# Optimization experiments

Hardware: AMD Instinct MI355X
Metric: run time of the kernel (lower is better)

The kernel has to match this reference:

```python
import jax, jax.numpy as jnp
import numpy as np

STEPS, K, NEW_PTS, GDIM, HDIM = 10, 64, 1152, 256, 128


def setup_inputs() -> dict:
    key = jax.random.key(0)
    ks = jax.random.split(key, 24)
    def w(k, shape):
        return jax.random.normal(k, shape, dtype=jnp.float32) * 0.02
    inp = {
        'points': jax.random.normal(ks[0], (4, 4096, 3), dtype=jnp.float32),
        'gt': jax.random.normal(ks[1], (4, 4096, 3), dtype=jnp.float32),
        # PointNet encoder: 3->64->128->256 (stored [in,out])
        'enc_w1': w(ks[2], (3, 64)),   'enc_b1': jnp.zeros((64,), jnp.float32),
        'enc_w2': w(ks[3], (64, 128)), 'enc_b2': jnp.zeros((128,), jnp.float32),
        'enc_w3': w(ks[4], (128, GDIM)), 'enc_b3': jnp.zeros((GDIM,), jnp.float32),
        # Attention MLP: (3+256+128)->128->1
        'att_w1': w(ks[5], (3 + GDIM + HDIM, 128)), 'att_b1': jnp.zeros((128,), jnp.float32),
        'att_w2': w(ks[6], (128, 1)), 'att_b2': jnp.zeros((1,), jnp.float32),
        # LSTMCell: input 256+3+3=262, hidden 128, gates i,f,g,o
        'lstm_wih': w(ks[7], (GDIM + 6, 4 * HDIM)), 'lstm_whh': w(ks[8], (HDIM, 4 * HDIM)),
        'lstm_bih': jnp.zeros((4 * HDIM,), jnp.float32), 'lstm_bhh': jnp.zeros((4 * HDIM,), jnp.float32),
        # Refiner: 128->128->new_points*3
        'ref_w1': w(ks[9], (HDIM, 128)), 'ref_b1': jnp.zeros((128,), jnp.float32),
        'ref_w2': w(ks[10], (128, NEW_PTS * 3)), 'ref_b2': jnp.zeros((NEW_PTS * 3,), jnp.float32),
    }
    return inp


def _chamfer_sq(x, y):
    # x: [B,N,3], y: [B,M,3]; squared-L2 chamfer, batch-mean (pytorch3d norm=2)
    d2 = (jnp.sum(x * x, -1)[:, :, None] + jnp.sum(y * y, -1)[:, None, :]
          - 2.0 * jnp.einsum('bnd,bmd->bnm', x, y))  # [B,N,M]
    cd = jnp.mean(jnp.min(d2, axis=2), axis=1) + jnp.mean(jnp.min(d2, axis=1), axis=1)
    return jnp.mean(cd)


def _forward(points, gt, enc_w1, enc_b1, enc_w2, enc_b2, enc_w3, enc_b3,
             att_w1, att_b1, att_w2, att_b2,
             lstm_wih, lstm_whh, lstm_bih, lstm_bhh,
             ref_w1, ref_b1, ref_w2, ref_b2):
    B, N0, _ = points.shape
    h = jnp.zeros((B, HDIM), points.dtype)
    c = jnp.zeros((B, HDIM), points.dtype)
    canvas = points
    for _ in range(STEPS):
        # PointNet encoder + max-pool -> global feature [B,GDIM]
        f = jax.nn.relu(canvas @ enc_w1 + enc_b1)
        f = jax.nn.relu(f @ enc_w2 + enc_b2)
        f = f @ enc_w3 + enc_b3
        gfeat = jnp.max(f, axis=1)
        # attention-weighted centroid
        N = canvas.shape[1]
        ctx = jnp.concatenate([
            canvas,
            jnp.broadcast_to(gfeat[:, None, :], (B, N, GDIM)),
            jnp.broadcast_to(h[:, None, :], (B, N, HDIM)),
        ], axis=-1)
        scores = (jax.nn.relu(ctx @ att_w1 + att_b1) @ att_w2 + att_b2)[..., 0]  # [B,N]
        alpha = jax.nn.softmax(scores, axis=1)
        center = jnp.einsum('bn,bnd->bd', alpha, canvas)
        # brute-force KNN around center + gather
        dist = jnp.linalg.norm(canvas - center[:, None, :], axis=-1)  # [B,N]
        _, idx = jax.lax.top_k(-dist, K)  # smallest K
        patch = jnp.take_along_axis(canvas, idx[:, :, None], axis=1)  # [B,K,3]
        patch_feat = jnp.mean(patch - center[:, None, :], axis=1)  # [B,3]
        # LSTM cell (gate order i,f,g,o)
        lstm_in = jnp.concatenate([gfeat, center, patch_feat], axis=1)
        gates = lstm_in @ lstm_wih + lstm_bih + h @ lstm_whh + lstm_bhh
        gi, gf, gg, go = jnp.split(gates, 4, axis=1)
        c = jax.nn.sigmoid(gf) * c + jax.nn.sigmoid(gi) * jnp.tanh(gg)
        h = jax.nn.sigmoid(go) * jnp.tanh(c)
        # refine: generate new patch points around center
        new_pts = (jax.nn.relu(h @ ref_w1 + ref_b1) @ ref_w2 + ref_b2)
        new_pts = new_pts.reshape(B, NEW_PTS, 3) * 0.02 + center[:, None, :]
        canvas = jnp.concatenate([canvas, new_pts], axis=1)
    p_input = canvas[:, :N0, :]
    p_new = canvas[:, N0:, :]
    total_loss = 0.1 * _chamfer_sq(p_input, gt) + 1.0 * _chamfer_sq(p_new, gt)
    return total_loss


def reference(points, gt, enc_w1, enc_b1, enc_w2, enc_b2, enc_w3, enc_b3,
              att_w1, att_b1, att_w2, att_b2,
              lstm_wih, lstm_whh, lstm_bih, lstm_bhh,
              ref_w1, ref_b1, ref_w2, ref_b2):
    return _forward(points, gt, enc_w1, enc_b1, enc_w2, enc_b2, enc_w3, enc_b3,
                    att_w1, att_b1, att_w2, att_b2,
                    lstm_wih, lstm_whh, lstm_bih, lstm_bhh,
                    ref_w1, ref_b1, ref_w2, ref_b2)
```

## Files before the change

### kernel.cpp

```cpp
#include <hip/hip_runtime.h>
#include <math.h>

#define BB 4
#define N0 4096
#define NEWP 1152
#define GD 256
#define HD 128
#define KSEL 64
#define NSTEPS 10
#define NMAX (N0 + NSTEPS*NEWP)
#define NNEW (NSTEPS*NEWP)
#define F2S (BB*N0)

#define OFF_CANVAS 0
#define OFF_MINAB  (OFF_CANVAS + BB*NMAX*3)
#define OFF_MINCD  (OFF_MINAB + 2*BB*N0)
#define OFF_GMAX   (OFF_MINCD + BB*NNEW + BB*N0)
#define OFF_H      (OFF_GMAX + BB*GD)
#define OFF_C      (OFF_H + 2*BB*HD)
#define OFF_ACC    (OFF_C + 2*BB*HD)
#define OFF_CENTER (OFF_ACC + 16)
#define OFF_PART   (OFF_CENTER + 32)
#define OFF_GPART  (OFF_PART + BB*32*8)
#define OFF_F2     (OFF_GPART + 32*BB*512)
#define WS_FLOATS  (OFF_F2 + 128*F2S)

__device__ __forceinline__ unsigned enc_f(float f){
  unsigned u = __float_as_uint(f);
  return (u & 0x80000000u) ? ~u : (u | 0x80000000u);
}
__device__ __forceinline__ float dec_f(unsigned e){
  unsigned u = (e & 0x80000000u) ? (e & 0x7fffffffu) : ~e;
  return __uint_as_float(u);
}
__device__ __forceinline__ float sigm(float x){ return 1.f/(1.f+expf(-x)); }

__device__ __forceinline__ float block_sum(float v, volatile float* red){
#pragma unroll
  for (int s=32;s>0;s>>=1) v += __shfl_down(v, s, 64);
  int lane = threadIdx.x & 63, w = threadIdx.x >> 6, nw = blockDim.x >> 6;
  __syncthreads();
  if (lane==0) red[w] = v;
  __syncthreads();
  if (w==0){
    float x = (lane < nw) ? red[lane] : 0.f;
#pragma unroll
    for (int s=8;s>0;s>>=1) x += __shfl_down(x, s, 64);
    if (lane==0) red[0] = x;
  }
  __syncthreads();
  float r = red[0];
  __syncthreads();
  return r;
}
__device__ __forceinline__ float block_max(float v, volatile float* red){
#pragma unroll
  for (int s=32;s>0;s>>=1) v = fmaxf(v, __shfl_down(v, s, 64));
  int lane = threadIdx.x & 63, w = threadIdx.x >> 6, nw = blockDim.x >> 6;
  __syncthreads();
  if (lane==0) red[w] = v;
  __syncthreads();
  if (w==0){
    float x = (lane < nw) ? red[lane] : -3.4e38f;
#pragma unroll
    for (int s=8;s>0;s>>=1) x = fmaxf(x, __shfl_down(x, s, 64));
    if (lane==0) red[0] = x;
  }
  __syncthreads();
  float r = red[0];
  __syncthreads();
  return r;
}

__global__ __launch_bounds__(512) void init_kernel(
    const float* __restrict__ points,
    float* __restrict__ canvas, unsigned* __restrict__ minAB,
    unsigned* __restrict__ minCD, unsigned* __restrict__ gmax,
    float* __restrict__ h, float* __restrict__ c)
{
  int gid = blockIdx.x*512 + threadIdx.x;
  if (gid < BB*N0*3){
    int b = gid/(N0*3), r = gid - b*(N0*3);
    canvas[(size_t)b*NMAX*3 + r] = points[gid];
  }
  if (gid < 2*BB*N0) minAB[gid] = 0xFFFFFFFFu;
  if (gid < BB*NNEW + BB*N0) minCD[gid] = 0xFFFFFFFFu;
  if (gid < BB*GD) gmax[gid] = 0u;
  if (gid < 2*BB*HD){ h[gid]=0.f; c[gid]=0.f; }
}

__global__ __launch_bounds__(256) void enc12_kernel(
    const float* __restrict__ canvas, const float* __restrict__ w1,
    const float* __restrict__ b1, const float* __restrict__ w2,
    const float* __restrict__ b2, float* __restrict__ f2buf,
    int off, int M)
{
  int b = blockIdx.y;
  int jc = blockIdx.z;
  int i = blockIdx.x*256 + threadIdx.x;
  int ii = (i < M) ? i : 0;
  const float* p = canvas + (size_t)(b*NMAX + off + ii)*3;
  float p0 = p[0], p1 = p[1], p2 = p[2];
  float f1[64];
#pragma unroll
  for (int j=0;j<64;j++)
    f1[j] = fmaxf(0.f, b1[j] + p0*w1[j] + p1*w1[64+j] + p2*w1[128+j]);
  float a[16];
  const float* b2p = b2 + jc*16;
#pragma unroll
  for (int j=0;j<16;j++) a[j] = b2p[j];
#pragma unroll
  for (int k=0;k<64;k++){
    const float* wr = w2 + k*128 + jc*16;
#pragma unroll
    for (int j=0;j<16;j++) a[j] = fmaf(f1[k], wr[j], a[j]);
  }
  if (i < M){
    int base = b*N0 + i;
#pragma unroll
    for (int j=0;j<16;j++)
      f2buf[(size_t)(jc*16 + j)*F2S + base] = fmaxf(a[j], 0.f);
  }
}

__global__ __launch_bounds__(256) void enc3_kernel(
    const float* __restrict__ f2buf, const float* __restrict__ w3,
    const float* __restrict__ b3, unsigned* __restrict__ gmax, int M)
{
  int b = blockIdx.y;
  int dc = blockIdx.z;
  int i = blockIdx.x*256 + threadIdx.x;
  bool act = i < M;
  int ii = act ? i : 0;
  const float* fp = f2buf + b*N0 + ii;
  float a[16];
  const float* b3p = b3 + dc*16;
#pragma unroll
  for (int d=0;d<16;d++) a[d] = b3p[d];
  for (int k=0;k<128;k++){
    float fk = fp[(size_t)k*F2S];
    const float* wr = w3 + k*256 + dc*16;
#pragma unroll
    for (int d=0;d<16;d++) a[d] = fmaf(fk, wr[d], a[d]);
  }
#pragma unroll
  for (int d=0;d<16;d++){
    float v = act ? a[d] : -3.4e38f;
#pragma unroll
    for (int s=32;s>0;s>>=1) v = fmaxf(v, __shfl_down(v, s, 64));
    if ((threadIdx.x & 63) == 0) atomicMax(&gmax[b*GD + dc*16 + d], enc_f(v));
  }
}

__global__ __launch_bounds__(512) void sl_kernel(
    const float* __restrict__ canvas, const float* __restrict__ aw1,
    const float* __restrict__ ab1, const float* __restrict__ aw2,
    const float* __restrict__ ab2, const unsigned* __restrict__ gmax,
    const float* __restrict__ h_in,
    const float* __restrict__ wih, const float* __restrict__ whh,
    float* __restrict__ part, float* __restrict__ gpart, int N, int nch)
{
  __shared__ float sBatt[128];
  __shared__ float red[16];
  __shared__ float sV[BB][12];
  int blk = blockIdx.x;
  int tid = threadIdx.x;
  if (blk < 4*nch){
    int b = blk / nch, ch = blk - b*nch;
    if (tid < 128){
      float a = ab1[tid];
      for (int k=0;k<GD;k++) a += dec_f(gmax[b*GD+k]) * aw1[(3+k)*128 + tid];
      for (int k=0;k<HD;k++) a += h_in[b*HD+k] * aw1[(3+GD+k)*128 + tid];
      sBatt[tid] = a;
    }
    __syncthreads();
    int i = ch*512 + tid;
    bool act = i < N;
    float p0=0.f,p1=0.f,p2=0.f,s=-3.4e38f;
    if (act){
      const float* pp = canvas + (size_t)(b*NMAX + i)*3;
      p0=pp[0]; p1=pp[1]; p2=pp[2];
      s = ab2[0];
      for (int j=0;j<128;j++){
        float v = sBatt[j] + p0*aw1[j] + p1*aw1[128+j] + p2*aw1[256+j];
        s += fmaxf(v, 0.f)*aw2[j];
      }
    }
    float mb = block_max(s, red);
    float e = act ? expf(s - mb) : 0.f;
    float se = block_sum(e, red);
    float wx = block_sum(e*p0, red);
    float wy = block_sum(e*p1, red);
    float wz = block_sum(e*p2, red);
    if (tid==0){
      float* pr = part + (size_t)(b*32 + ch)*8;
      pr[0]=mb; pr[1]=se; pr[2]=wx; pr[3]=wy; pr[4]=wz;
    }
  } else {
    int cc = blk - 4*nch;
    if (tid < BB*12){
      int b = tid/12, j = tid - b*12;
      int r = cc*12 + j;
      sV[b][j] = (r < 256) ? dec_f(gmax[b*GD + r]) : h_in[b*HD + (r-256)];
    }
    __syncthreads();
    float a0=0.f,a1=0.f,a2=0.f,a3=0.f;
#pragma unroll
    for (int j=0;j<12;j++){
      int r = cc*12 + j;
      const float* wr = (r < 256) ? (wih + (size_t)r*512) : (whh + (size_t)(r-256)*512);
      float wvv = wr[tid];
      a0 += sV[0][j]*wvv; a1 += sV[1][j]*wvv;
      a2 += sV[2][j]*wvv; a3 += sV[3][j]*wvv;
    }
    float* gp = gpart + (size_t)cc*(BB*512);
    gp[0*512+tid]=a0; gp[1*512+tid]=a1; gp[2*512+tid]=a2; gp[3*512+tid]=a3;
  }
}

__global__ __launch_bounds__(1024) void stepA_kernel(
    const float* __restrict__ canvas, const float* __restrict__ part,
    float* __restrict__ centerpf, int N, int nch)
{
  __shared__ float red[16];
  __shared__ float sC[3];
  __shared__ unsigned cbufA[2][16];
  __shared__ unsigned cbufB[2][16];
  __shared__ int tieCnt;
  __shared__ int tieIdx[256];

  int b = blockIdx.x;
  int tid = threadIdx.x;
  int lane = tid & 63, wid = tid >> 6;
  const float* cv = canvas + (size_t)b*NMAX*3;

  float pm=-3.4e38f, pse=0.f, pwx=0.f, pwy=0.f, pwz=0.f;
  if (tid < nch){
    const float* pp = part + (size_t)(b*32 + tid)*8;
    pm=pp[0]; pse=pp[1]; pwx=pp[2]; pwy=pp[3]; pwz=pp[4];
  }
  float M = block_max(pm, red);
  float w = (tid < nch) ? expf(pm - M) : 0.f;
  float se = block_sum(pse*w, red);
  float wx = block_sum(pwx*w, red);
  float wy = block_sum(pwy*w, red);
  float wz = block_sum(pwz*w, red);
  if (tid==0){ sC[0]=wx/se; sC[1]=wy/se; sC[2]=wz/se; }
  __syncthreads();
  float cx=sC[0], cy=sC[1], cz=sC[2];
  if (tid<3) centerpf[b*3+tid] = sC[tid];

  unsigned ur[16];
#pragma unroll
  for (int q=0;q<16;q++){
    ur[q] = 0xFFFFFFFFu;
    int i = tid + q*1024;
    if (i < N){
      const float* p = cv + (size_t)i*3;
      float dx=p[0]-cx, dy=p[1]-cy, dz=p[2]-cz;
      ur[q] = __float_as_uint(dx*dx + dy*dy + dz*dz);
    }
  }

  unsigned T = 0u;
  int cntBelow = 0;
  int par = 0;
  {
    unsigned cand = 1u<<30;
    unsigned tc = 0;
#pragma unroll
    for (int q=0;q<16;q++) tc += (ur[q] < cand) ? 1u : 0u;
#pragma unroll
    for (int s=32;s>0;s>>=1) tc += __shfl_down(tc, s, 64);
    if (lane==0) cbufA[par][wid] = tc;
    __syncthreads();
    unsigned tot = 0;
#pragma unroll
    for (int i2=0;i2<16;i2++) tot += cbufA[par][i2];
    if ((int)tot < KSEL){ T = cand; cntBelow = (int)tot; }
    par ^= 1;
  }
  for (int bit=29; bit>=1; bit-=2){
    unsigned q1 = 1u<<(bit-1);
    unsigned c1 = T + q1, c2 = T + 2u*q1, c3 = T + 3u*q1;
    unsigned ta = 0, tb = 0;
#pragma unroll
    for (int q=0;q<16;q++){
      unsigned u = ur[q];
      ta += (u < c1 ? 1u : 0u) | (u < c2 ? 0x10000u : 0u);
      tb += (u < c3 ? 1u : 0u);
    }
#pragma unroll
    for (int s=32;s>0;s>>=1){ ta += __shfl_down(ta, s, 64); tb += __shfl_down(tb, s, 64); }
    if (lane==0){ cbufA[par][wid] = ta; cbufB[par][wid] = tb; }
    __syncthreads();
    unsigned sa = 0, sb = 0;
#pragma unroll
    for (int i2=0;i2<16;i2++){ sa += cbufA[par][i2]; sb += cbufB[par][i2]; }
    int n1 = (int)(sa & 0xFFFFu), n2 = (int)(sa >> 16), n3 = (int)sb;
    if (n3 < KSEL){ T = c3; cntBelow = n3; }
    else if (n2 < KSEL){ T = c2; cntBelow = n2; }
    else if (n1 < KSEL){ T = c1; cntBelow = n1; }
    par ^= 1;
  }
  int kneed = KSEL - cntBelow;

  if (tid==0) tieCnt = 0;
  __syncthreads();
  float sx=0.f, sy=0.f, sz=0.f;
#pragma unroll
  for (int q=0;q<16;q++){
    unsigned u = ur[q];
    if (u < T){
      const float* p = cv + (size_t)(tid + q*1024)*3;
      sx += p[0]; sy += p[1]; sz += p[2];
    } else if (u == T){
      int pos = atomicAdd(&tieCnt, 1);
      if (pos < 256) tieIdx[pos] = tid + q*1024;
    }
  }
  __syncthreads();
  sx = block_sum(sx, red);
  sy = block_sum(sy, red);
  sz = block_sum(sz, red);
  if (tid==0){
    int mm = tieCnt < 256 ? tieCnt : 256;
    for (int t=0;t<kneed;t++){
      int best=-1, bi=0x7fffffff;
      for (int q=0;q<mm;q++){ int v = tieIdx[q]; if (v < bi){ bi=v; best=q; } }
      if (best >= 0){
        tieIdx[best] = 0x7fffffff;
        const float* p = cv + (size_t)bi*3;
        sx += p[0]; sy += p[1]; sz += p[2];
      }
    }
    centerpf[16 + b*3 + 0] = sx/KSEL - cx;
    centerpf[16 + b*3 + 1] = sy/KSEL - cy;
    centerpf[16 + b*3 + 2] = sz/KSEL - cz;
  }
}

__global__ __launch_bounds__(256) void refine_kernel(
    float* __restrict__ canvas, const float* __restrict__ gpart,
    const float* __restrict__ centerpf,
    const float* __restrict__ c_in, float* __restrict__ c_out,
    float* __restrict__ h_out,
    const float* __restrict__ wih,
    const float* __restrict__ bih, const float* __restrict__ bhh,
    const float* __restrict__ rw1, const float* __restrict__ rb1,
    const float* __restrict__ rw2, const float* __restrict__ rb2, int N)
{
  __shared__ float sG[512];
  __shared__ float sH[HD];
  __shared__ float sRf[HD];
  int g = blockIdx.x, b = blockIdx.y;
  int tid = threadIdx.x;
  float cx = centerpf[b*3+0], cy = centerpf[b*3+1], cz = centerpf[b*3+2];
  float fx = centerpf[16+b*3+0], fy = centerpf[16+b*3+1], fz = centerpf[16+b*3+2];
#pragma unroll
  for (int half=0; half<2; half++){
    int o = tid + half*256;
    float gg = bih[o] + bhh[o];
    for (int cc=0; cc<32; cc++) gg += gpart[(size_t)cc*(BB*512) + b*512 + o];
    gg += cx*wih[(size_t)256*512+o] + cy*wih[(size_t)257*512+o] + cz*wih[(size_t)258*512+o];
    gg += fx*wih[(size_t)259*512+o] + fy*wih[(size_t)260*512+o] + fz*wih[(size_t)261*512+o];
    sG[o] = gg;
  }
  __syncthreads();
  if (tid < HD){
    float gi=sG[tid], gf=sG[128+tid], gg2=sG[256+tid], go=sG[384+tid];
    float cn = sigm(gf)*c_in[b*HD+tid] + sigm(gi)*tanhf(gg2);
    float hn = sigm(go)*tanhf(cn);
    sH[tid] = hn;
    if (g==0){ c_out[b*HD+tid]=cn; h_out[b*HD+tid]=hn; }
  }
  __syncthreads();
  if (tid < HD){
    float a = rb1[tid];
    for (int k=0;k<HD;k++) a += sH[k]*rw1[k*HD + tid];
    sRf[tid] = fmaxf(a, 0.f);
  }
  __syncthreads();
  int o = g*256 + tid;
  if (o < NEWP*3){
    float a = rb2[o];
    for (int k=0;k<HD;k++) a += sRf[k]*rw2[(size_t)k*(NEWP*3) + o];
    canvas[((size_t)b*NMAX + N)*3 + o] = a*0.02f + centerpf[b*3 + (o%3)];
  }
}

__global__ __launch_bounds__(512) void chamfer_kernel(
    const float* __restrict__ canvas, const float* __restrict__ gt,
    unsigned* __restrict__ minAB, unsigned* __restrict__ minCD)
{
  __shared__ float sy0[1024], sy1[1024], sy2[1024], sny[1024];
  int id = blockIdx.x;
  int dir, rem;
  if (id < 32){ dir=0; rem=id; }
  else if (id < 64){ dir=1; rem=id-32; }
  else if (id < 160){ dir=2; rem=id-64; }
  else { dir=3; rem=id-160; }
  int b, xb, yb;
  if (dir < 2){ b = rem>>3; int l = rem&7; xb = l>>2; yb = l&3; }
  else if (dir == 2){ b = rem/24; int l = rem%24; xb = l>>2; yb = l&3; }
  else { b = rem/24; int l = rem%24; xb = l/12; yb = l%12; }

  int Nx, Ny; const float* X; const float* Y; unsigned* mp;
  if (dir==0){      Nx=N0;   Ny=N0;   X=canvas+(size_t)b*NMAX*3;       Y=gt+(size_t)b*N0*3;            mp=minAB + b*N0; }
  else if (dir==1){ Nx=N0;   Ny=N0;   X=gt+(size_t)b*N0*3;             Y=canvas+(size_t)b*NMAX*3;      mp=minAB + BB*N0 + b*N0; }
  else if (dir==2){ Nx=NNEW; Ny=N0;   X=canvas+((size_t)b*NMAX+N0)*3;  Y=gt+(size_t)b*N0*3;            mp=minCD + b*NNEW; }
  else {            Nx=N0;   Ny=NNEW; X=gt+(size_t)b*N0*3;             Y=canvas+((size_t)b*NMAX+N0)*3; mp=minCD + BB*NNEW + b*N0; }

  int xbase = xb*2048;
  int ybase = yb*1024;
  int tn = min(1024, Ny - ybase);
  int tid = threadIdx.x;
  for (int t=tid; t<tn; t+=512){
    const float* yp = Y + (size_t)(ybase+t)*3;
    float y0=yp[0], y1=yp[1], y2=yp[2];
    sy0[t]=-2.f*y0; sy1[t]=-2.f*y1; sy2[t]=-2.f*y2; sny[t]=y0*y0+y1*y1+y2*y2;
  }
  __syncthreads();

  float X0[4],X1[4],X2[4],NXr[4],MN[4]; int XI[4]; bool VA[4];
#pragma unroll
  for (int q=0;q<4;q++){
    int x = xbase + q*512 + tid;
    VA[q] = x < Nx;
    int xc = VA[q] ? x : 0;
    const float* xp = X + (size_t)xc*3;
    X0[q]=xp[0]; X1[q]=xp[1]; X2[q]=xp[2];
    NXr[q] = X0[q]*X0[q] + X1[q]*X1[q] + X2[q]*X2[q];
    MN[q] = 3.4e38f; XI[q] = xc;
  }
  const float4* v0 = (const float4*)sy0;
  const float4* v1 = (const float4*)sy1;
  const float4* v2 = (const float4*)sy2;
  const float4* vn = (const float4*)sny;
  int j4n = tn >> 2;
  for (int j=0;j<j4n;j++){
    float4 a0 = v0[j], a1 = v1[j], a2 = v2[j], an = vn[j];
#pragma unroll
    for (int e=0;e<4;e++){
      float y0 = ((const float*)&a0)[e];
      float y1 = ((const float*)&a1)[e];
      float y2 = ((const float*)&a2)[e];
      float ny = ((const float*)&an)[e];
#pragma unroll
      for (int q=0;q<4;q++){
        float d = fmaf(X0[q], y0, fmaf(X1[q], y1, fmaf(X2[q], y2, ny)));
        MN[q] = fminf(MN[q], d);
      }
    }
  }
  for (int j=j4n*4; j<tn; j++){
    float y0=sy0[j], y1=sy1[j], y2=sy2[j], ny=sny[j];
#pragma unroll
    for (int q=0;q<4;q++){
      float d = fmaf(X0[q], y0, fmaf(X1[q], y1, fmaf(X2[q], y2, ny)));
      MN[q] = fminf(MN[q], d);
    }
  }
#pragma unroll
  for (int q=0;q<4;q++)
    if (VA[q]) atomicMin(&mp[XI[q]], enc_f(MN[q] + NXr[q]));
}

__global__ __launch_bounds__(256) void chamfer_reduce_kernel(
    const unsigned* __restrict__ minAB, const unsigned* __restrict__ minCD,
    float* __restrict__ acc)
{
  __shared__ float red[16];
  int s = blockIdx.x, dir = s>>2, b = s&3;
  const unsigned* mp; int len;
  if (dir==0){      mp=minAB + b*N0;            len=N0; }
  else if (dir==1){ mp=minAB + BB*N0 + b*N0;    len=N0; }
  else if (dir==2){ mp=minCD + b*NNEW;          len=NNEW; }
  else {            mp=minCD + BB*NNEW + b*N0;  len=N0; }
  float v = 0.f;
  for (int i=threadIdx.x;i<len;i+=256) v += dec_f(mp[i]);
  v = block_sum(v, red);
  if (threadIdx.x==0) acc[s] = v;
}

__global__ void finish_kernel(const float* __restrict__ acc, float* __restrict__ out)
{
  if (threadIdx.x == 0 && blockIdx.x == 0){
    float cd1 = 0.f, cd2 = 0.f;
    for (int b=0;b<BB;b++) cd1 += acc[b]/(float)N0 + acc[4+b]/(float)N0;
    for (int b=0;b<BB;b++) cd2 += acc[8+b]/(float)NNEW + acc[12+b]/(float)N0;
    out[0] = 0.1f*(cd1/BB) + 1.0f*(cd2/BB);
  }
}

extern "C" void kernel_launch(void* const* d_in, const int* in_sizes, int n_in,
                              void* d_out, int out_size, void* d_ws, size_t ws_size,
                              hipStream_t stream) {
  (void)in_sizes; (void)n_in; (void)out_size; (void)ws_size;
  const float* points   = (const float*)d_in[0];
  const float* gt       = (const float*)d_in[1];
  const float* enc_w1   = (const float*)d_in[2];
  const float* enc_b1   = (const float*)d_in[3];
  const float* enc_w2   = (const float*)d_in[4];
  const float* enc_b2   = (const float*)d_in[5];
  const float* enc_w3   = (const float*)d_in[6];
  const float* enc_b3   = (const float*)d_in[7];
  const float* att_w1   = (const float*)d_in[8];
  const float* att_b1   = (const float*)d_in[9];
  const float* att_w2   = (const float*)d_in[10];
  const float* att_b2   = (const float*)d_in[11];
  const float* lstm_wih = (const float*)d_in[12];
  const float* lstm_whh = (const float*)d_in[13];
  const float* lstm_bih = (const float*)d_in[14];
  const float* lstm_bhh = (const float*)d_in[15];
  const float* ref_w1   = (const float*)d_in[16];
  const float* ref_b1   = (const float*)d_in[17];
  const float* ref_w2   = (const float*)d_in[18];
  const float* ref_b2   = (const float*)d_in[19];
  float* out = (float*)d_out;

  float* ws       = (float*)d_ws;
  float* canvas   = ws + OFF_CANVAS;
  unsigned* minAB = (unsigned*)(ws + OFF_MINAB);
  unsigned* minCD = (unsigned*)(ws + OFF_MINCD);
  unsigned* gmaxp = (unsigned*)(ws + OFF_GMAX);
  float* hb       = ws + OFF_H;
  float* cb       = ws + OFF_C;
  float* acc      = ws + OFF_ACC;
  float* centerb  = ws + OFF_CENTER;
  float* partb    = ws + OFF_PART;
  float* gpartb   = ws + OFF_GPART;
  float* f2buf    = ws + OFF_F2;

  init_kernel<<<dim3(128), 512, 0, stream>>>(points, canvas, minAB, minCD, gmaxp, hb, cb);
  enc12_kernel<<<dim3(16, BB, 8), 256, 0, stream>>>(canvas, enc_w1, enc_b1, enc_w2, enc_b2, f2buf, 0, N0);
  enc3_kernel<<<dim3(16, BB, 16), 256, 0, stream>>>(f2buf, enc_w3, enc_b3, gmaxp, N0);

  for (int t=0; t<NSTEPS; t++){
    int N   = N0 + t*NEWP;
    int nch = (N + 511) >> 9;
    float* h_in  = hb + (t&1)*BB*HD;
    float* h_out = hb + ((t+1)&1)*BB*HD;
    float* c_in  = cb + (t&1)*BB*HD;
    float* c_out = cb + ((t+1)&1)*BB*HD;
    sl_kernel<<<dim3(4*nch + 32), 512, 0, stream>>>(canvas, att_w1, att_b1, att_w2, att_b2,
                                                    gmaxp, h_in, lstm_wih, lstm_whh,
                                                    partb, gpartb, N, nch);
    stepA_kernel<<<dim3(BB), 1024, 0, stream>>>(canvas, partb, centerb, N, nch);
    refine_kernel<<<dim3(14, BB), 256, 0, stream>>>(canvas, gpartb, centerb,
                                                    c_in, c_out, h_out,
                                                    lstm_wih, lstm_bih, lstm_bhh,
                                                    ref_w1, ref_b1, ref_w2, ref_b2, N);
    if (t < NSTEPS-1){
      enc12_kernel<<<dim3(5, BB, 8), 256, 0, stream>>>(canvas, enc_w1, enc_b1, enc_w2, enc_b2, f2buf, N, NEWP);
      enc3_kernel<<<dim3(5, BB, 16), 256, 0, stream>>>(f2buf, enc_w3, enc_b3, gmaxp, NEWP);
    }
  }

  chamfer_kernel<<<dim3(256), 512, 0, stream>>>(canvas, gt, minAB, minCD);
  chamfer_reduce_kernel<<<dim3(16), 256, 0, stream>>>(minAB, minCD, acc);
  finish_kernel<<<1, 64, 0, stream>>>(acc, out);
}
```

Before: 1.061 ms.

## Fuse refine with encoder layers 1-2 and template stepA on point count

The refine kernel now also runs encoder layers 1 and 2 on the points it generates, writing f2buf directly and removing a separate enc12 launch per step. Each block recomputes the LSTM gates and the refiner MLP redundantly across 8 channel chunks, so that compute is repeated. stepA is templated on the number of points per thread, so early steps with small N keep fewer registers and run fewer loop iterations. On the last step the fused kernel still computes the encoder features even though nothing uses them.

```diff
diff --git a/kernel.cpp b/kernel.cpp
--- a/kernel.cpp
+++ b/kernel.cpp
@@ -218,6 +218,7 @@
   }
 }
 
+template<int Q>
 __global__ __launch_bounds__(1024) void stepA_kernel(
     const float* __restrict__ canvas, const float* __restrict__ part,
     float* __restrict__ centerpf, int N, int nch)
@@ -250,9 +251,9 @@
   float cx=sC[0], cy=sC[1], cz=sC[2];
   if (tid<3) centerpf[b*3+tid] = sC[tid];
 
-  unsigned ur[16];
-#pragma unroll
-  for (int q=0;q<16;q++){
+  unsigned ur[Q];
+#pragma unroll
+  for (int q=0;q<Q;q++){
     ur[q] = 0xFFFFFFFFu;
     int i = tid + q*1024;
     if (i < N){
@@ -269,7 +270,7 @@
     unsigned cand = 1u<<30;
     unsigned tc = 0;
 #pragma unroll
-    for (int q=0;q<16;q++) tc += (ur[q] < cand) ? 1u : 0u;
+    for (int q=0;q<Q;q++) tc += (ur[q] < cand) ? 1u : 0u;
 #pragma unroll
     for (int s=32;s>0;s>>=1) tc += __shfl_down(tc, s, 64);
     if (lane==0) cbufA[par][wid] = tc;
@@ -285,7 +286,7 @@
     unsigned c1 = T + q1, c2 = T + 2u*q1, c3 = T + 3u*q1;
     unsigned ta = 0, tb = 0;
 #pragma unroll
-    for (int q=0;q<16;q++){
+    for (int q=0;q<Q;q++){
       unsigned u = ur[q];
       ta += (u < c1 ? 1u : 0u) | (u < c2 ? 0x10000u : 0u);
       tb += (u < c3 ? 1u : 0u);
@@ -309,7 +310,7 @@
   __syncthreads();
   float sx=0.f, sy=0.f, sz=0.f;
 #pragma unroll
-  for (int q=0;q<16;q++){
+  for (int q=0;q<Q;q++){
     unsigned u = ur[q];
     if (u < T){
       const float* p = cv + (size_t)(tid + q*1024)*3;
@@ -340,7 +341,7 @@
   }
 }
 
-__global__ __launch_bounds__(256) void refine_kernel(
+__global__ __launch_bounds__(256) void refenc12_kernel(
     float* __restrict__ canvas, const float* __restrict__ gpart,
     const float* __restrict__ centerpf,
     const float* __restrict__ c_in, float* __restrict__ c_out,
@@ -348,12 +349,16 @@
     const float* __restrict__ wih,
     const float* __restrict__ bih, const float* __restrict__ bhh,
     const float* __restrict__ rw1, const float* __restrict__ rb1,
-    const float* __restrict__ rw2, const float* __restrict__ rb2, int N)
+    const float* __restrict__ rw2, const float* __restrict__ rb2,
+    const float* __restrict__ w1, const float* __restrict__ b1,
+    const float* __restrict__ w2, const float* __restrict__ b2,
+    float* __restrict__ f2buf, int N)
 {
   __shared__ float sG[512];
   __shared__ float sH[HD];
   __shared__ float sRf[HD];
-  int g = blockIdx.x, b = blockIdx.y;
+  int b = blockIdx.y;
+  int jc = blockIdx.z;
   int tid = threadIdx.x;
   float cx = centerpf[b*3+0], cy = centerpf[b*3+1], cz = centerpf[b*3+2];
   float fx = centerpf[16+b*3+0], fy = centerpf[16+b*3+1], fz = centerpf[16+b*3+2];
@@ -372,7 +377,7 @@
     float cn = sigm(gf)*c_in[b*HD+tid] + sigm(gi)*tanhf(gg2);
     float hn = sigm(go)*tanhf(cn);
     sH[tid] = hn;
-    if (g==0){ c_out[b*HD+tid]=cn; h_out[b*HD+tid]=hn; }
+    if (blockIdx.x==0 && jc==0){ c_out[b*HD+tid]=cn; h_out[b*HD+tid]=hn; }
   }
   __syncthreads();
   if (tid < HD){
@@ -381,11 +386,39 @@
     sRf[tid] = fmaxf(a, 0.f);
   }
   __syncthreads();
-  int o = g*256 + tid;
-  if (o < NEWP*3){
-    float a = rb2[o];
-    for (int k=0;k<HD;k++) a += sRf[k]*rw2[(size_t)k*(NEWP*3) + o];
-    canvas[((size_t)b*NMAX + N)*3 + o] = a*0.02f + centerpf[b*3 + (o%3)];
+  int i = blockIdx.x*256 + tid;
+  bool act = i < NEWP;
+  int ic = act ? i : 0;
+  float a0 = rb2[3*ic], a1 = rb2[3*ic+1], a2 = rb2[3*ic+2];
+  for (int k=0;k<HD;k++){
+    const float* wv = rw2 + (size_t)k*(NEWP*3) + 3*ic;
+    float hk = sRf[k];
+    a0 = fmaf(hk, wv[0], a0); a1 = fmaf(hk, wv[1], a1); a2 = fmaf(hk, wv[2], a2);
+  }
+  float p0 = fmaf(a0, 0.02f, cx), p1 = fmaf(a1, 0.02f, cy), p2 = fmaf(a2, 0.02f, cz);
+  if (act && jc==0){
+    float* cp = canvas + ((size_t)b*NMAX + N + i)*3;
+    cp[0]=p0; cp[1]=p1; cp[2]=p2;
+  }
+  float f1[64];
+#pragma unroll
+  for (int j=0;j<64;j++)
+    f1[j] = fmaxf(0.f, b1[j] + p0*w1[j] + p1*w1[64+j] + p2*w1[128+j]);
+  float a[16];
+  const float* b2p = b2 + jc*16;
+#pragma unroll
+  for (int j=0;j<16;j++) a[j] = b2p[j];
+#pragma unroll
+  for (int k=0;k<64;k++){
+    const float* wr = w2 + k*128 + jc*16;
+#pragma unroll
+    for (int j=0;j<16;j++) a[j] = fmaf(f1[k], wr[j], a[j]);
+  }
+  if (act){
+    int base = b*N0 + i;
+#pragma unroll
+    for (int j=0;j<16;j++)
+      f2buf[(size_t)(jc*16 + j)*F2S + base] = fmaxf(a[j], 0.f);
   }
 }
 
@@ -546,13 +579,17 @@
     sl_kernel<<<dim3(4*nch + 32), 512, 0, stream>>>(canvas, att_w1, att_b1, att_w2, att_b2,
                                                     gmaxp, h_in, lstm_wih, lstm_whh,
                                                     partb, gpartb, N, nch);
-    stepA_kernel<<<dim3(BB), 1024, 0, stream>>>(canvas, partb, centerb, N, nch);
-    refine_kernel<<<dim3(14, BB), 256, 0, stream>>>(canvas, gpartb, centerb,
-                                                    c_in, c_out, h_out,
-                                                    lstm_wih, lstm_bih, lstm_bhh,
-                                                    ref_w1, ref_b1, ref_w2, ref_b2, N);
+    if      (N <= 4096)  stepA_kernel<4> <<<dim3(BB), 1024, 0, stream>>>(canvas, partb, centerb, N, nch);
+    else if (N <= 8192)  stepA_kernel<8> <<<dim3(BB), 1024, 0, stream>>>(canvas, partb, centerb, N, nch);
+    else if (N <= 12288) stepA_kernel<12><<<dim3(BB), 1024, 0, stream>>>(canvas, partb, centerb, N, nch);
+    else                 stepA_kernel<16><<<dim3(BB), 1024, 0, stream>>>(canvas, partb, centerb, N, nch);
+    refenc12_kernel<<<dim3(5, BB, 8), 256, 0, stream>>>(canvas, gpartb, centerb,
+                                                        c_in, c_out, h_out,
+                                                        lstm_wih, lstm_bih, lstm_bhh,
+                                                        ref_w1, ref_b1, ref_w2, ref_b2,
+                                                        enc_w1, enc_b1, enc_w2, enc_b2,
+                                                        f2buf, N);
     if (t < NSTEPS-1){
-      enc12_kernel<<<dim3(5, BB, 8), 256, 0, stream>>>(canvas, enc_w1, enc_b1, enc_w2, enc_b2, f2buf, N, NEWP);
       enc3_kernel<<<dim3(5, BB, 16), 256, 0, stream>>>(f2buf, enc_w3, enc_b3, gmaxp, NEWP);
     }
   }
```

Result: faster. 1.035 ms (-2.5%).
